# Kernel optimization log

Measured on AMD Instinct MI355X. Metric: run time of the kernel, lower is better.

Reference implementation:

```python
import jax, jax.numpy as jnp
import numpy as np

DIMS, HEAD, FREQ = 1024, 16, 10000
HEAD_DIM = DIMS // HEAD          # 64
ROT = HEAD_DIM // 2              # 32
B, S = 4, 8192


def setup_inputs() -> dict:
    key = jax.random.key(0)
    k1, k2, k3, k4 = jax.random.split(key, 4)
    x = jax.random.normal(k1, (B, S, DIMS), dtype=jnp.float32)
    matrix = jax.random.normal(k2, (HEAD_DIM, HEAD_DIM), dtype=jnp.float32)
    thetas = jax.random.normal(k3, (ROT,), dtype=jnp.float32) * 0.1
    tscale = jnp.ones((1,), dtype=jnp.float32)
    # inverse frequencies exactly as in __init__
    invf = (1.0 / FREQ ** (jnp.arange(0, HEAD_DIM, 2, dtype=jnp.float32) / HEAD_DIM)).astype(jnp.float32)
    pairs = jax.random.randint(k4, (ROT, 2), 0, HEAD_DIM, dtype=jnp.int32)
    return {"x": x, "matrix": matrix, "thetas": thetas, "tscale": tscale,
            "invf": invf, "pairs": pairs}


def _composed_rotation(thetas, tscale, pairs, d, dtype):
    # Build every Givens matrix G_k (same element-set order as the torch code)
    theta = thetas * tscale[0]

    def make_G(i, j, th):
        c, sn = jnp.cos(th), jnp.sin(th)
        G = jnp.eye(d, dtype=dtype)
        return G.at[i, i].set(c).at[j, j].set(c).at[i, j].set(-sn).at[j, i].set(sn)

    Gs = jax.vmap(make_G)(pairs[:, 0], pairs[:, 1], theta)  # [rot, d, d]

    def step(acc, G):
        return acc @ G, None

    G_comb, _ = jax.lax.scan(step, jnp.eye(d, dtype=dtype), Gs)
    return G_comb


def reference(x, matrix, thetas, tscale, invf, pairs):
    b, s, dims = x.shape
    d = matrix.shape[0]          # head_dim
    h = dims // d                # heads

    G_comb = _composed_rotation(thetas, tscale, pairs, d, x.dtype)

    xr = x.reshape(b, s, h, d)
    # flat @ G_combined @ self.matrix (acts on last dim)
    xr = xr @ (G_comb @ matrix)

    # sinusoidal RoPE: sinusoid[s, d/2] = pos * invf
    pos = jnp.arange(s, dtype=x.dtype)
    sinusoid = pos[:, None] * invf[None, :]
    sin = jnp.sin(sinusoid)[None, :, None, :]   # [1, s, 1, d/2]
    cos = jnp.cos(sinusoid)[None, :, None, :]

    x1, x2 = xr[..., ::2], xr[..., 1::2]
    out = jnp.concatenate([x1 * cos - x2 * sin, x1 * sin + x2 * cos], axis=-1)
    return out.reshape(b, s, dims) * jnp.asarray(np.sqrt(dims), x.dtype)
```

## Files before the change

### kernel.cpp

```cpp
#include <hip/hip_runtime.h>
#include <math.h>

#define BB 4
#define SS 8192
#define HH 16
#define DD 64
#define ROT 32
#define NG (BB * SS * HH)
#define RPB 128
#define LSTR 65
#define TPB 512
#define NBLK 512
#define TILES (NG / (RPB * NBLK))

typedef float f32x4 __attribute__((ext_vector_type(4)));

__global__ void setup_GM(const float* __restrict__ thetas,
                         const float* __restrict__ tscale,
                         const int* __restrict__ pairs,
                         const float* __restrict__ matrix,
                         float* __restrict__ M) {
  __shared__ float Gs[DD][DD];
  const int t = threadIdx.x;
  if (t < DD) {
    for (int c = 0; c < DD; ++c) Gs[t][c] = (t == c) ? 1.0f : 0.0f;
    const float ts = tscale[0];
    for (int r = 0; r < ROT; ++r) {
      const int i = pairs[2 * r], j = pairs[2 * r + 1];
      const float th = thetas[r] * ts;
      const float cc = cosf(th), sn = sinf(th);
      if (i == j) {
        Gs[t][i] *= sn;
      } else {
        const float a = Gs[t][i], b = Gs[t][j];
        Gs[t][i] = a * cc + b * sn;
        Gs[t][j] = b * cc - a * sn;
      }
    }
  }
  __syncthreads();
  const int e = blockIdx.x * 256 + t;
  const int row = e >> 6, col = e & 63;
  float a0 = 0.f, a1 = 0.f, a2 = 0.f, a3 = 0.f;
  for (int k = 0; k < DD; k += 4) {
    a0 = fmaf(Gs[row][k], matrix[k * DD + col], a0);
    a1 = fmaf(Gs[row][k + 1], matrix[(k + 1) * DD + col], a1);
    a2 = fmaf(Gs[row][k + 2], matrix[(k + 2) * DD + col], a2);
    a3 = fmaf(Gs[row][k + 3], matrix[(k + 3) * DD + col], a3);
  }
  M[e] = (a0 + a1) + (a2 + a3);
}

__global__ void setup_table(const float* __restrict__ invf,
                            float* __restrict__ tab) {
  const int idx = blockIdx.x * 256 + threadIdx.x;
  if (idx >= SS * 32) return;
  const int s = idx >> 5, d = idx & 31;
  const float ang = (float)s * invf[d];
  tab[s * 64 + d] = 32.0f * cosf(ang);
  tab[s * 64 + 32 + d] = 32.0f * sinf(ang);
}

__global__ __launch_bounds__(TPB, 4) void apply_rot(
    const float* __restrict__ x, const float* __restrict__ M,
    const float* __restrict__ tab, const float* __restrict__ invf,
    float* __restrict__ out) {
  __shared__ float lds[2][RPB * LSTR];
  const int tid = threadIdx.x;
  const int r = tid & (RPB - 1);
  const int h = __builtin_amdgcn_readfirstlane(tid >> 7);
  const float* __restrict__ Mh = M + h * 16;

  const size_t tile0 = (size_t)blockIdx.x * TILES;

  {
    const float4* __restrict__ xg = (const float4*)x + tile0 * (RPB * 16);
#pragma unroll
    for (int i = 0; i < 4; ++i) {
      const int f = i * TPB + tid;
      *(float4*)&lds[0][(f >> 4) * LSTR + (f & 15) * 4] = xg[f];
    }
  }
  __syncthreads();

  int p = 0;
#pragma unroll 1
  for (int t = 0; t < TILES; ++t) {
    const size_t tile = tile0 + t;

    float4 st0, st1, st2, st3;
    if (t + 1 < TILES) {
      const float4* __restrict__ xg =
          (const float4*)x + (tile + 1) * (RPB * 16);
      st0 = xg[0 * TPB + tid];
      st1 = xg[1 * TPB + tid];
      st2 = xg[2 * TPB + tid];
      st3 = xg[3 * TPB + tid];
    }

    const float* __restrict__ xr = &lds[p][r * LSTR];
    float acc[16];
#pragma unroll
    for (int c = 0; c < 16; ++c) acc[c] = 0.0f;

#pragma unroll 4
    for (int k4 = 0; k4 < 16; ++k4) {
      const float4 xv = *(const float4*)&xr[k4 * 4];
      const float* __restrict__ m0 = Mh + k4 * 4 * DD;
#pragma unroll
      for (int c = 0; c < 16; ++c) acc[c] = fmaf(xv.x, m0[c], acc[c]);
#pragma unroll
      for (int c = 0; c < 16; ++c) acc[c] = fmaf(xv.y, m0[DD + c], acc[c]);
#pragma unroll
      for (int c = 0; c < 16; ++c) acc[c] = fmaf(xv.z, m0[2 * DD + c], acc[c]);
#pragma unroll
      for (int c = 0; c < 16; ++c) acc[c] = fmaf(xv.w, m0[3 * DD + c], acc[c]);
    }

    const int g = (int)(tile * RPB) + r;
    const int spos = (g >> 4) & (SS - 1);
    float cz[8], sz[8];
    if (tab) {
      const float4* __restrict__ tc = (const float4*)(tab + spos * 64 + h * 8);
      const float4* __restrict__ tn =
          (const float4*)(tab + spos * 64 + 32 + h * 8);
#pragma unroll
      for (int q = 0; q < 2; ++q) {
        *(float4*)&cz[4 * q] = tc[q];
        *(float4*)&sz[4 * q] = tn[q];
      }
    } else {
#pragma unroll
      for (int d = 0; d < 8; ++d) {
        const float ang = (float)spos * invf[h * 8 + d];
        cz[d] = 32.0f * cosf(ang);
        sz[d] = 32.0f * sinf(ang);
      }
    }

    float4 lov[2], hiv[2];
#pragma unroll
    for (int q = 0; q < 2; ++q) {
#pragma unroll
      for (int d = 0; d < 4; ++d) {
        const int dd = 4 * q + d;
        const float e = acc[2 * dd], o = acc[2 * dd + 1];
        ((float*)&lov[q])[d] = e * cz[dd] - o * sz[dd];
        ((float*)&hiv[q])[d] = e * sz[dd] + o * cz[dd];
      }
    }

    __syncthreads();

    float* __restrict__ orow = &lds[p][r * LSTR];
#pragma unroll
    for (int q = 0; q < 2; ++q) {
      *(float4*)&orow[8 * h + 4 * q] = lov[q];
      *(float4*)&orow[32 + 8 * h + 4 * q] = hiv[q];
    }
    if (t + 1 < TILES) {
      float* __restrict__ nb = lds[p ^ 1];
      {
        const int f = 0 * TPB + tid;
        *(float4*)&nb[(f >> 4) * LSTR + (f & 15) * 4] = st0;
      }
      {
        const int f = 1 * TPB + tid;
        *(float4*)&nb[(f >> 4) * LSTR + (f & 15) * 4] = st1;
      }
      {
        const int f = 2 * TPB + tid;
        *(float4*)&nb[(f >> 4) * LSTR + (f & 15) * 4] = st2;
      }
      {
        const int f = 3 * TPB + tid;
        *(float4*)&nb[(f >> 4) * LSTR + (f & 15) * 4] = st3;
      }
    }
    __syncthreads();

    float4* __restrict__ og = (float4*)out + tile * (RPB * 16);
#pragma unroll
    for (int i = 0; i < 4; ++i) {
      const int f = i * TPB + tid;
      const float4 v = *(const float4*)&lds[p][(f >> 4) * LSTR + (f & 15) * 4];
      __builtin_nontemporal_store(*(const f32x4*)&v, (f32x4*)&og[f]);
    }
    p ^= 1;
  }
}

extern "C" void kernel_launch(void* const* d_in, const int* in_sizes, int n_in,
                              void* d_out, int out_size, void* d_ws,
                              size_t ws_size, hipStream_t stream) {
  const float* x = (const float*)d_in[0];
  const float* matrix = (const float*)d_in[1];
  const float* thetas = (const float*)d_in[2];
  const float* tscale = (const float*)d_in[3];
  const float* invf = (const float*)d_in[4];
  const int* pairs = (const int*)d_in[5];
  float* out = (float*)d_out;

  float* M = (float*)d_ws;
  float* tab = M + DD * DD;
  const size_t need = (size_t)(DD * DD + SS * 64) * sizeof(float);
  const bool have_tab = ws_size >= need;

  setup_GM<<<16, 256, 0, stream>>>(thetas, tscale, pairs, matrix, M);
  if (have_tab) setup_table<<<(SS * 32) / 256, 256, 0, stream>>>(invf, tab);
  apply_rot<<<NBLK, TPB, 0, stream>>>(x, M, have_tab ? tab : nullptr, invf,
                                      out);
}
```

Before: 296.8 us.

## Single-buffer LDS tile, double block count, and hoist RoPE table loads

Replaces the double-buffered LDS tile with a single buffer, which halves the shared-memory footprint. The launch bound rises to 8 blocks per CU and the grid to 1024 blocks. The RoPE cos/sin table loads move ahead of the matmul so their latency overlaps the compute, and the LDS addresses are precomputed once. In exchange, each tile needs an extra barrier, because the next tile can only be written after the current output has been read back from LDS. The higher occupancy target also tightens register limits and may cause spills.

```diff
diff --git a/kernel.cpp b/kernel.cpp
--- a/kernel.cpp
+++ b/kernel.cpp
@@ -10,7 +10,7 @@
 #define RPB 128
 #define LSTR 65
 #define TPB 512
-#define NBLK 512
+#define NBLK 1024
 #define TILES (NG / (RPB * NBLK))
 
 typedef float f32x4 __attribute__((ext_vector_type(4)));
@@ -61,34 +61,52 @@
   tab[s * 64 + 32 + d] = 32.0f * sinf(ang);
 }
 
-__global__ __launch_bounds__(TPB, 4) void apply_rot(
+__global__ __launch_bounds__(TPB, 8) void apply_rot(
     const float* __restrict__ x, const float* __restrict__ M,
     const float* __restrict__ tab, const float* __restrict__ invf,
     float* __restrict__ out) {
-  __shared__ float lds[2][RPB * LSTR];
+  __shared__ float lds[RPB * LSTR];
   const int tid = threadIdx.x;
   const int r = tid & (RPB - 1);
   const int h = __builtin_amdgcn_readfirstlane(tid >> 7);
   const float* __restrict__ Mh = M + h * 16;
-
   const size_t tile0 = (size_t)blockIdx.x * TILES;
+
+  int fa[4];
+#pragma unroll
+  for (int i = 0; i < 4; ++i) {
+    const int f = i * TPB + tid;
+    fa[i] = (f >> 4) * LSTR + (f & 15) * 4;
+  }
 
   {
     const float4* __restrict__ xg = (const float4*)x + tile0 * (RPB * 16);
-#pragma unroll
-    for (int i = 0; i < 4; ++i) {
-      const int f = i * TPB + tid;
-      *(float4*)&lds[0][(f >> 4) * LSTR + (f & 15) * 4] = xg[f];
-    }
+    const float4 s0 = xg[0 * TPB + tid], s1 = xg[1 * TPB + tid],
+                 s2 = xg[2 * TPB + tid], s3 = xg[3 * TPB + tid];
+    *(float4*)&lds[fa[0]] = s0;
+    *(float4*)&lds[fa[1]] = s1;
+    *(float4*)&lds[fa[2]] = s2;
+    *(float4*)&lds[fa[3]] = s3;
   }
   __syncthreads();
 
-  int p = 0;
+  float4 st0, st1, st2, st3;
 #pragma unroll 1
   for (int t = 0; t < TILES; ++t) {
     const size_t tile = tile0 + t;
-
-    float4 st0, st1, st2, st3;
+    const int g = (int)(tile * RPB) + r;
+    const int spos = (g >> 4) & (SS - 1);
+
+    float cz[8], sz[8];
+    if (tab) {
+      const float4* __restrict__ tc = (const float4*)(tab + spos * 64 + h * 8);
+      const float4* __restrict__ tn =
+          (const float4*)(tab + spos * 64 + 32 + h * 8);
+      *(float4*)&cz[0] = tc[0];
+      *(float4*)&cz[4] = tc[1];
+      *(float4*)&sz[0] = tn[0];
+      *(float4*)&sz[4] = tn[1];
+    }
     if (t + 1 < TILES) {
       const float4* __restrict__ xg =
           (const float4*)x + (tile + 1) * (RPB * 16);
@@ -98,7 +116,7 @@
       st3 = xg[3 * TPB + tid];
     }
 
-    const float* __restrict__ xr = &lds[p][r * LSTR];
+    const float* __restrict__ xr = &lds[r * LSTR];
     float acc[16];
 #pragma unroll
     for (int c = 0; c < 16; ++c) acc[c] = 0.0f;
@@ -117,19 +135,7 @@
       for (int c = 0; c < 16; ++c) acc[c] = fmaf(xv.w, m0[3 * DD + c], acc[c]);
     }
 
-    const int g = (int)(tile * RPB) + r;
-    const int spos = (g >> 4) & (SS - 1);
-    float cz[8], sz[8];
-    if (tab) {
-      const float4* __restrict__ tc = (const float4*)(tab + spos * 64 + h * 8);
-      const float4* __restrict__ tn =
-          (const float4*)(tab + spos * 64 + 32 + h * 8);
-#pragma unroll
-      for (int q = 0; q < 2; ++q) {
-        *(float4*)&cz[4 * q] = tc[q];
-        *(float4*)&sz[4 * q] = tn[q];
-      }
-    } else {
+    if (!tab) {
 #pragma unroll
       for (int d = 0; d < 8; ++d) {
         const float ang = (float)spos * invf[h * 8 + d];
@@ -152,41 +158,28 @@
 
     __syncthreads();
 
-    float* __restrict__ orow = &lds[p][r * LSTR];
-#pragma unroll
-    for (int q = 0; q < 2; ++q) {
-      *(float4*)&orow[8 * h + 4 * q] = lov[q];
-      *(float4*)&orow[32 + 8 * h + 4 * q] = hiv[q];
+    float* __restrict__ orow = &lds[r * LSTR];
+    *(float4*)&orow[8 * h + 0] = lov[0];
+    *(float4*)&orow[8 * h + 4] = lov[1];
+    *(float4*)&orow[32 + 8 * h + 0] = hiv[0];
+    *(float4*)&orow[32 + 8 * h + 4] = hiv[1];
+
+    __syncthreads();
+
+    float4* __restrict__ og = (float4*)out + tile * (RPB * 16);
+#pragma unroll
+    for (int i = 0; i < 4; ++i) {
+      const float4 v = *(const float4*)&lds[fa[i]];
+      __builtin_nontemporal_store(*(const f32x4*)&v,
+                                  (f32x4*)&og[i * TPB + tid]);
     }
     if (t + 1 < TILES) {
-      float* __restrict__ nb = lds[p ^ 1];
-      {
-        const int f = 0 * TPB + tid;
-        *(float4*)&nb[(f >> 4) * LSTR + (f & 15) * 4] = st0;
-      }
-      {
-        const int f = 1 * TPB + tid;
-        *(float4*)&nb[(f >> 4) * LSTR + (f & 15) * 4] = st1;
-      }
-      {
-        const int f = 2 * TPB + tid;
-        *(float4*)&nb[(f >> 4) * LSTR + (f & 15) * 4] = st2;
-      }
-      {
-        const int f = 3 * TPB + tid;
-        *(float4*)&nb[(f >> 4) * LSTR + (f & 15) * 4] = st3;
-      }
+      *(float4*)&lds[fa[0]] = st0;
+      *(float4*)&lds[fa[1]] = st1;
+      *(float4*)&lds[fa[2]] = st2;
+      *(float4*)&lds[fa[3]] = st3;
     }
     __syncthreads();
-
-    float4* __restrict__ og = (float4*)out + tile * (RPB * 16);
-#pragma unroll
-    for (int i = 0; i < 4; ++i) {
-      const int f = i * TPB + tid;
-      const float4 v = *(const float4*)&lds[p][(f >> 4) * LSTR + (f & 15) * 4];
-      __builtin_nontemporal_store(*(const f32x4*)&v, (f32x4*)&og[f]);
-    }
-    p ^= 1;
   }
 }
 
```

After: 320.8 us. 8.1% more time.
